# Performance work log

Hardware: AMD Instinct MI355X
Metric: run time of the kernel (lower is better)

Reference implementation:

```python
import jax, jax.numpy as jnp
import numpy as np

B, T, C, D = 4, 2048, 1024, 64


def setup_inputs() -> dict:
    key = jax.random.key(0)
    k_x, k_wq, k_wk, k_wv, k_b = jax.random.split(key, 5)
    s = 1.0 / np.sqrt(C)
    return {
        "hidden_states": jax.random.normal(k_x, (B, T, C), dtype=jnp.float32),
        "w_q": jax.random.normal(k_wq, (C, D), dtype=jnp.float32) * s,
        "w_k": jax.random.normal(k_wk, (C, D), dtype=jnp.float32) * s,
        "w_v": jax.random.normal(k_wv, (C, D), dtype=jnp.float32) * s,
        "b_q": jnp.zeros((D,), dtype=jnp.float32),
        "b_k": jnp.zeros((D,), dtype=jnp.float32),
        "b_v": jnp.zeros((D,), dtype=jnp.float32),
    }


def reference(hidden_states, w_q, w_k, w_v, b_q, b_k, b_v):
    # Single causal self-attention head (dropout = 0 / eval mode).
    q = hidden_states @ w_q + b_q                      # (B, T, D)
    k = hidden_states @ w_k + b_k                      # (B, T, D)
    v = hidden_states @ w_v + b_v                      # (B, T, D)
    scores = jnp.einsum("btd,bsd->bts", q, k) / jnp.sqrt(jnp.float32(D))
    t = hidden_states.shape[1]
    causal = jnp.tril(jnp.ones((t, t), dtype=bool))    # (T, T)
    scores = jnp.where(causal, scores, jnp.float32(-jnp.inf))
    weights = jax.nn.softmax(scores, axis=-1)          # (B, T, T)
    return jnp.einsum("bts,bsd->btd", weights, v)      # (B, T, D)
```

## Files before the change

### kernel.cpp

```cpp
#include <hip/hip_runtime.h>
#include <hip/hip_bf16.h>

constexpr int Bn = 4;
constexpr int Tn = 2048;
constexpr int Cn = 1024;
constexpr int Dn = 64;

typedef __attribute__((ext_vector_type(8))) short short8;
typedef __attribute__((ext_vector_type(4))) float f32x4;

__device__ inline short f2bf(float f) {
    unsigned u = __builtin_bit_cast(unsigned, f);
    u += 0x7FFFu + ((u >> 16) & 1u);
    return (short)(u >> 16);
}

__global__ __launch_bounds__(256) void prep_w(
    const float* __restrict__ wq, const float* __restrict__ wk,
    const float* __restrict__ wv, short* __restrict__ wt)
{
    const int sel = blockIdx.x >> 4;
    const float* w = sel == 0 ? wq : (sel == 1 ? wk : wv);
    short* o = wt + (size_t)sel * Dn * Cn;
    const int base = (blockIdx.x & 15) * 4096;
    for (int idx = base + threadIdx.x; idx < base + 4096; idx += 256) {
        int n = idx >> 10, k = idx & 1023;
        o[idx] = f2bf(w[k * Dn + n]);
    }
}

__global__ __launch_bounds__(64) void qkv_mfma(
    const float* __restrict__ x, const short* __restrict__ wt,
    const float* __restrict__ bq, const float* __restrict__ bk,
    const float* __restrict__ bv,
    short* __restrict__ Qbf, short* __restrict__ Kbf, short* __restrict__ Vt)
{
    const int l = threadIdx.x;
    const int i = l & 15, g = l >> 4;
    const int rowbase = blockIdx.x * 16;
    const int sel = blockIdx.y;

    const short* ws   = wt + (size_t)sel * Dn * Cn;
    const float* bias = sel == 0 ? bq : (sel == 1 ? bk : bv);

    f32x4 acc[4];
    #pragma unroll
    for (int nt = 0; nt < 4; ++nt)
        #pragma unroll
        for (int r = 0; r < 4; ++r) acc[nt][r] = 0.f;

    const float* xrow = x + (size_t)(rowbase + i) * Cn;

    for (int k0 = 0; k0 < Cn; k0 += 32) {
        float4 x0 = *reinterpret_cast<const float4*>(xrow + k0 + 8 * g);
        float4 x1 = *reinterpret_cast<const float4*>(xrow + k0 + 8 * g + 4);
        short8 af;
        af[0] = f2bf(x0.x); af[1] = f2bf(x0.y); af[2] = f2bf(x0.z); af[3] = f2bf(x0.w);
        af[4] = f2bf(x1.x); af[5] = f2bf(x1.y); af[6] = f2bf(x1.z); af[7] = f2bf(x1.w);
        #pragma unroll
        for (int nt = 0; nt < 4; ++nt) {
            short8 bf = *reinterpret_cast<const short8*>(
                ws + (size_t)(nt * 16 + i) * Cn + k0 + 8 * g);
            acc[nt] = __builtin_amdgcn_mfma_f32_16x16x32_bf16(af, bf, acc[nt], 0, 0, 0);
        }
    }

    #pragma unroll
    for (int r = 0; r < 4; ++r) {
        const int rho = rowbase + 4 * g + r;
        const int b = rho >> 11, t = rho & (Tn - 1);
        #pragma unroll
        for (int nt = 0; nt < 4; ++nt) {
            const int n = nt * 16 + i;
            const float val = acc[nt][r] + bias[n];
            if (sel == 0)      Qbf[(size_t)rho * Dn + n] = f2bf(val * 0.125f);
            else if (sel == 1) Kbf[(size_t)rho * Dn + n] = f2bf(val);
            else               Vt[((size_t)b * Dn + n) * Tn + t] = f2bf(val);
        }
    }
}

__global__ __launch_bounds__(256) void attn_fused(
    const short* __restrict__ Qbf, const short* __restrict__ Kbf,
    const short* __restrict__ Vt, float* __restrict__ out)
{
    __shared__ __align__(16) short Plds[4][16][72];
    __shared__ float o_part[4][16][68];
    __shared__ float ml_part[4][2][16];

    const int tid = threadIdx.x;
    const int w = tid >> 6, l = tid & 63;
    const int i = l & 15, g = l >> 4;
    const int b = blockIdx.y;
    const int qw = blockIdx.x * 16;

    const short* Qb = Qbf + (size_t)b * Tn * Dn;
    const short* Kb = Kbf + (size_t)b * Tn * Dn;
    const short* Vb = Vt + (size_t)b * Dn * Tn;

    short8 qf0 = *reinterpret_cast<const short8*>(Qb + (size_t)(qw + i) * Dn + 8 * g);
    short8 qf1 = *reinterpret_cast<const short8*>(Qb + (size_t)(qw + i) * Dn + 32 + 8 * g);

    f32x4 o4[4];
    f32x4 m, lsum;
    #pragma unroll
    for (int r = 0; r < 4; ++r) { m[r] = -1e30f; lsum[r] = 0.f; }
    #pragma unroll
    for (int dt = 0; dt < 4; ++dt)
        #pragma unroll
        for (int r = 0; r < 4; ++r) o4[dt][r] = 0.f;

    const int nch = (qw + 79) >> 6;
    for (int kb = w; kb < nch; kb += 4) {
        const int K0 = kb * 64;

        f32x4 s[4];
        #pragma unroll
        for (int nt = 0; nt < 4; ++nt)
            #pragma unroll
            for (int r = 0; r < 4; ++r) s[nt][r] = 0.f;
        #pragma unroll
        for (int nt = 0; nt < 4; ++nt) {
            const short* kr = Kb + (size_t)(K0 + nt * 16 + i) * Dn + 8 * g;
            short8 kf0 = *reinterpret_cast<const short8*>(kr);
            short8 kf1 = *reinterpret_cast<const short8*>(kr + 32);
            s[nt] = __builtin_amdgcn_mfma_f32_16x16x32_bf16(qf0, kf0, s[nt], 0, 0, 0);
            s[nt] = __builtin_amdgcn_mfma_f32_16x16x32_bf16(qf1, kf1, s[nt], 0, 0, 0);
        }

        if (K0 + 63 > qw) {
            #pragma unroll
            for (int nt = 0; nt < 4; ++nt)
                #pragma unroll
                for (int r = 0; r < 4; ++r) {
                    if (K0 + nt * 16 + i > qw + 4 * g + r) s[nt][r] = -1e30f;
                }
        }

        f32x4 rm;
        #pragma unroll
        for (int r = 0; r < 4; ++r)
            rm[r] = fmaxf(fmaxf(s[0][r], s[1][r]), fmaxf(s[2][r], s[3][r]));
        #pragma unroll
        for (int msk = 1; msk < 16; msk <<= 1)
            #pragma unroll
            for (int r = 0; r < 4; ++r) rm[r] = fmaxf(rm[r], __shfl_xor(rm[r], msk));

        f32x4 scl;
        #pragma unroll
        for (int r = 0; r < 4; ++r) {
            float mn = fmaxf(m[r], rm[r]);
            scl[r] = __expf(m[r] - mn);
            m[r] = mn;
            lsum[r] *= scl[r];
        }
        #pragma unroll
        for (int dt = 0; dt < 4; ++dt)
            #pragma unroll
            for (int r = 0; r < 4; ++r) o4[dt][r] *= scl[r];

        f32x4 rs;
        #pragma unroll
        for (int r = 0; r < 4; ++r) rs[r] = 0.f;
        #pragma unroll
        for (int nt = 0; nt < 4; ++nt)
            #pragma unroll
            for (int r = 0; r < 4; ++r) {
                float p = __expf(s[nt][r] - m[r]);
                rs[r] += p;
                Plds[w][4 * g + r][nt * 16 + i] = f2bf(p);
            }
        #pragma unroll
        for (int msk = 1; msk < 16; msk <<= 1)
            #pragma unroll
            for (int r = 0; r < 4; ++r) rs[r] += __shfl_xor(rs[r], msk);
        #pragma unroll
        for (int r = 0; r < 4; ++r) lsum[r] += rs[r];

        asm volatile("s_waitcnt lgkmcnt(0)" ::: "memory");
        __builtin_amdgcn_sched_barrier(0);

        short8 pf0 = *reinterpret_cast<const short8*>(&Plds[w][i][8 * g]);
        short8 pf1 = *reinterpret_cast<const short8*>(&Plds[w][i][32 + 8 * g]);
        #pragma unroll
        for (int dt = 0; dt < 4; ++dt) {
            const short* vr = Vb + (size_t)(dt * 16 + i) * Tn + K0 + 8 * g;
            short8 vf0 = *reinterpret_cast<const short8*>(vr);
            short8 vf1 = *reinterpret_cast<const short8*>(vr + 32);
            o4[dt] = __builtin_amdgcn_mfma_f32_16x16x32_bf16(pf0, vf0, o4[dt], 0, 0, 0);
            o4[dt] = __builtin_amdgcn_mfma_f32_16x16x32_bf16(pf1, vf1, o4[dt], 0, 0, 0);
        }
    }

    #pragma unroll
    for (int dt = 0; dt < 4; ++dt)
        #pragma unroll
        for (int r = 0; r < 4; ++r)
            o_part[w][4 * g + r][dt * 16 + i] = o4[dt][r];
    if (i == 0) {
        #pragma unroll
        for (int r = 0; r < 4; ++r) {
            ml_part[w][0][4 * g + r] = m[r];
            ml_part[w][1][4 * g + r] = lsum[r];
        }
    }
    __syncthreads();

    #pragma unroll
    for (int r = 0; r < 4; ++r) {
        const int row = 4 * g + r;
        float m0 = ml_part[0][0][row], m1 = ml_part[1][0][row];
        float m2 = ml_part[2][0][row], m3 = ml_part[3][0][row];
        float M = fmaxf(fmaxf(m0, m1), fmaxf(m2, m3));
        float w0 = __expf(m0 - M), w1 = __expf(m1 - M);
        float w2 = __expf(m2 - M), w3 = __expf(m3 - M);
        float L = ml_part[0][1][row] * w0 + ml_part[1][1][row] * w1 +
                  ml_part[2][1][row] * w2 + ml_part[3][1][row] * w3;
        float O = o_part[0][row][w * 16 + i] * w0 + o_part[1][row][w * 16 + i] * w1 +
                  o_part[2][row][w * 16 + i] * w2 + o_part[3][row][w * 16 + i] * w3;
        out[((size_t)b * Tn + qw + row) * Dn + w * 16 + i] = O / L;
    }
}

extern "C" void kernel_launch(void* const* d_in, const int* in_sizes, int n_in,
                              void* d_out, int out_size, void* d_ws, size_t ws_size,
                              hipStream_t stream) {
    const float* x  = (const float*)d_in[0];
    const float* wq = (const float*)d_in[1];
    const float* wk = (const float*)d_in[2];
    const float* wv = (const float*)d_in[3];
    const float* bq = (const float*)d_in[4];
    const float* bk = (const float*)d_in[5];
    const float* bv = (const float*)d_in[6];
    float* out = (float*)d_out;

    short* wt  = (short*)d_ws;
    short* Qbf = wt + 3 * Dn * Cn;
    short* Kbf = Qbf + (size_t)Bn * Tn * Dn;
    short* Vt  = Kbf + (size_t)Bn * Tn * Dn;

    prep_w<<<48, 256, 0, stream>>>(wq, wk, wv, wt);
    qkv_mfma<<<dim3((Bn * Tn) / 16, 3), 64, 0, stream>>>(x, wt, bq, bk, bv, Qbf, Kbf, Vt);
    attn_fused<<<dim3(Tn / 16, Bn), 256, 0, stream>>>(Qbf, Kbf, Vt, out);
}
```

Baseline: 149.5 us.

## Pre-convert activations to bf16, split QKV over N, use 8 waves in attention

Adds a prep pass that converts the full hidden_states tensor to bf16 in a workspace buffer, so the QKV projection loads bf16 directly instead of converting fp32 per block. The QKV kernel gets a third grid dimension that splits the 64 output columns into two halves, doubling the block count. The attention kernel goes from 4 to 8 waves per block, each wave taking a strided share of key chunks, and merges 8 partial softmax states at the end. The bf16 copy costs an extra full read and write of x, and the 8-way split doubles shared memory use per block and adds merge work.

```diff
diff --git a/kernel.cpp b/kernel.cpp
--- a/kernel.cpp
+++ b/kernel.cpp
@@ -15,22 +15,38 @@
     return (short)(u >> 16);
 }
 
-__global__ __launch_bounds__(256) void prep_w(
+__global__ __launch_bounds__(256) void prep(
+    const float* __restrict__ x,
     const float* __restrict__ wq, const float* __restrict__ wk,
-    const float* __restrict__ wv, short* __restrict__ wt)
+    const float* __restrict__ wv,
+    short* __restrict__ wt, short* __restrict__ xbf)
 {
-    const int sel = blockIdx.x >> 4;
-    const float* w = sel == 0 ? wq : (sel == 1 ? wk : wv);
-    short* o = wt + (size_t)sel * Dn * Cn;
-    const int base = (blockIdx.x & 15) * 4096;
-    for (int idx = base + threadIdx.x; idx < base + 4096; idx += 256) {
-        int n = idx >> 10, k = idx & 1023;
-        o[idx] = f2bf(w[k * Dn + n]);
+    if (blockIdx.x < 48) {
+        const int sel = blockIdx.x >> 4;
+        const float* w = sel == 0 ? wq : (sel == 1 ? wk : wv);
+        short* o = wt + (size_t)sel * Dn * Cn;
+        const int base = (blockIdx.x & 15) * 4096;
+        for (int idx = base + threadIdx.x; idx < base + 4096; idx += 256) {
+            int n = idx >> 10, k = idx & 1023;
+            o[idx] = f2bf(w[k * Dn + n]);
+        }
+    } else {
+        const int idx = (blockIdx.x - 48) * 256 + threadIdx.x;
+        const float4* xf = reinterpret_cast<const float4*>(x);
+        short8* xo = reinterpret_cast<short8*>(xbf);
+        constexpr int NU = Bn * Tn * Cn / 8;
+        for (int u = idx; u < NU; u += 262144) {
+            float4 a = xf[2 * u], c = xf[2 * u + 1];
+            short8 o;
+            o[0] = f2bf(a.x); o[1] = f2bf(a.y); o[2] = f2bf(a.z); o[3] = f2bf(a.w);
+            o[4] = f2bf(c.x); o[5] = f2bf(c.y); o[6] = f2bf(c.z); o[7] = f2bf(c.w);
+            xo[u] = o;
+        }
     }
 }
 
 __global__ __launch_bounds__(64) void qkv_mfma(
-    const float* __restrict__ x, const short* __restrict__ wt,
+    const short* __restrict__ xbf, const short* __restrict__ wt,
     const float* __restrict__ bq, const float* __restrict__ bk,
     const float* __restrict__ bv,
     short* __restrict__ Qbf, short* __restrict__ Kbf, short* __restrict__ Vt)
@@ -39,30 +55,27 @@
     const int i = l & 15, g = l >> 4;
     const int rowbase = blockIdx.x * 16;
     const int sel = blockIdx.y;
+    const int nh = blockIdx.z;
 
     const short* ws   = wt + (size_t)sel * Dn * Cn;
     const float* bias = sel == 0 ? bq : (sel == 1 ? bk : bv);
 
-    f32x4 acc[4];
-    #pragma unroll
-    for (int nt = 0; nt < 4; ++nt)
-        #pragma unroll
-        for (int r = 0; r < 4; ++r) acc[nt][r] = 0.f;
-
-    const float* xrow = x + (size_t)(rowbase + i) * Cn;
+    f32x4 acc[2];
+    #pragma unroll
+    for (int nt2 = 0; nt2 < 2; ++nt2)
+        #pragma unroll
+        for (int r = 0; r < 4; ++r) acc[nt2][r] = 0.f;
+
+    const short* xrow = xbf + (size_t)(rowbase + i) * Cn + 8 * g;
+    const short* wb0  = ws + (size_t)(nh * 32 + i) * Cn + 8 * g;
+    const short* wb1  = wb0 + (size_t)16 * Cn;
 
     for (int k0 = 0; k0 < Cn; k0 += 32) {
-        float4 x0 = *reinterpret_cast<const float4*>(xrow + k0 + 8 * g);
-        float4 x1 = *reinterpret_cast<const float4*>(xrow + k0 + 8 * g + 4);
-        short8 af;
-        af[0] = f2bf(x0.x); af[1] = f2bf(x0.y); af[2] = f2bf(x0.z); af[3] = f2bf(x0.w);
-        af[4] = f2bf(x1.x); af[5] = f2bf(x1.y); af[6] = f2bf(x1.z); af[7] = f2bf(x1.w);
-        #pragma unroll
-        for (int nt = 0; nt < 4; ++nt) {
-            short8 bf = *reinterpret_cast<const short8*>(
-                ws + (size_t)(nt * 16 + i) * Cn + k0 + 8 * g);
-            acc[nt] = __builtin_amdgcn_mfma_f32_16x16x32_bf16(af, bf, acc[nt], 0, 0, 0);
-        }
+        short8 af = *reinterpret_cast<const short8*>(xrow + k0);
+        short8 b0 = *reinterpret_cast<const short8*>(wb0 + k0);
+        short8 b1 = *reinterpret_cast<const short8*>(wb1 + k0);
+        acc[0] = __builtin_amdgcn_mfma_f32_16x16x32_bf16(af, b0, acc[0], 0, 0, 0);
+        acc[1] = __builtin_amdgcn_mfma_f32_16x16x32_bf16(af, b1, acc[1], 0, 0, 0);
     }
 
     #pragma unroll
@@ -70,9 +83,9 @@
         const int rho = rowbase + 4 * g + r;
         const int b = rho >> 11, t = rho & (Tn - 1);
         #pragma unroll
-        for (int nt = 0; nt < 4; ++nt) {
-            const int n = nt * 16 + i;
-            const float val = acc[nt][r] + bias[n];
+        for (int nt2 = 0; nt2 < 2; ++nt2) {
+            const int n = (nh * 2 + nt2) * 16 + i;
+            const float val = acc[nt2][r] + bias[n];
             if (sel == 0)      Qbf[(size_t)rho * Dn + n] = f2bf(val * 0.125f);
             else if (sel == 1) Kbf[(size_t)rho * Dn + n] = f2bf(val);
             else               Vt[((size_t)b * Dn + n) * Tn + t] = f2bf(val);
@@ -80,13 +93,13 @@
     }
 }
 
-__global__ __launch_bounds__(256) void attn_fused(
+__global__ __launch_bounds__(512) void attn_fused(
     const short* __restrict__ Qbf, const short* __restrict__ Kbf,
     const short* __restrict__ Vt, float* __restrict__ out)
 {
-    __shared__ __align__(16) short Plds[4][16][72];
-    __shared__ float o_part[4][16][68];
-    __shared__ float ml_part[4][2][16];
+    __shared__ __align__(16) short Plds[8][16][72];
+    __shared__ float o_part[8][16][68];
+    __shared__ float ml_part[8][2][16];
 
     const int tid = threadIdx.x;
     const int w = tid >> 6, l = tid & 63;
@@ -111,7 +124,7 @@
         for (int r = 0; r < 4; ++r) o4[dt][r] = 0.f;
 
     const int nch = (qw + 79) >> 6;
-    for (int kb = w; kb < nch; kb += 4) {
+    for (int kb = w; kb < nch; kb += 8) {
         const int K0 = kb * 64;
 
         f32x4 s[4];
@@ -206,19 +219,22 @@
     }
     __syncthreads();
 
-    #pragma unroll
-    for (int r = 0; r < 4; ++r) {
-        const int row = 4 * g + r;
-        float m0 = ml_part[0][0][row], m1 = ml_part[1][0][row];
-        float m2 = ml_part[2][0][row], m3 = ml_part[3][0][row];
-        float M = fmaxf(fmaxf(m0, m1), fmaxf(m2, m3));
-        float w0 = __expf(m0 - M), w1 = __expf(m1 - M);
-        float w2 = __expf(m2 - M), w3 = __expf(m3 - M);
-        float L = ml_part[0][1][row] * w0 + ml_part[1][1][row] * w1 +
-                  ml_part[2][1][row] * w2 + ml_part[3][1][row] * w3;
-        float O = o_part[0][row][w * 16 + i] * w0 + o_part[1][row][w * 16 + i] * w1 +
-                  o_part[2][row][w * 16 + i] * w2 + o_part[3][row][w * 16 + i] * w3;
-        out[((size_t)b * Tn + qw + row) * Dn + w * 16 + i] = O / L;
+    if (w < 4) {
+        #pragma unroll
+        for (int r = 0; r < 4; ++r) {
+            const int row = 4 * g + r;
+            float M = -1e30f;
+            #pragma unroll
+            for (int p = 0; p < 8; ++p) M = fmaxf(M, ml_part[p][0][row]);
+            float L = 0.f, O = 0.f;
+            #pragma unroll
+            for (int p = 0; p < 8; ++p) {
+                float wp = __expf(ml_part[p][0][row] - M);
+                L += ml_part[p][1][row] * wp;
+                O += o_part[p][row][w * 16 + i] * wp;
+            }
+            out[((size_t)b * Tn + qw + row) * Dn + w * 16 + i] = O / L;
+        }
     }
 }
 
@@ -235,11 +251,13 @@
     float* out = (float*)d_out;
 
     short* wt  = (short*)d_ws;
-    short* Qbf = wt + 3 * Dn * Cn;
+    short* xbf = wt + 3 * Dn * Cn;
+    short* Qbf = xbf + (size_t)Bn * Tn * Cn;
     short* Kbf = Qbf + (size_t)Bn * Tn * Dn;
     short* Vt  = Kbf + (size_t)Bn * Tn * Dn;
 
-    prep_w<<<48, 256, 0, stream>>>(wq, wk, wv, wt);
-    qkv_mfma<<<dim3((Bn * Tn) / 16, 3), 64, 0, stream>>>(x, wt, bq, bk, bv, Qbf, Kbf, Vt);
-    attn_fused<<<dim3(Tn / 16, Bn), 256, 0, stream>>>(Qbf, Kbf, Vt, out);
-}
+    prep<<<1072, 256, 0, stream>>>(x, wq, wk, wv, wt, xbf);
+    qkv_mfma<<<dim3((Bn * Tn) / 16, 3, 2), 64, 0, stream>>>(
+        xbf, wt, bq, bk, bv, Qbf, Kbf, Vt);
+    attn_fused<<<dim3(Tn / 16, Bn), 512, 0, stream>>>(Qbf, Kbf, Vt, out);
+}
```

Result: slower. 156.2 us (+4.5%).

## Prefetch x in QKV projection, hoist V loads, and use 8 waves in attention

Applied to the files above, without the earlier changes.

The QKV projection kernel now double-buffers its fp32 input loads two k-steps ahead and fully unrolls the k loop, so global loads can overlap the MFMA work. The attention kernel doubles its block to 8 waves, giving each wave fewer key chunks. V fragments are loaded right after the QK MFMAs so their latency overlaps the softmax. The final merge now combines 8 partial results, with only the first 4 waves writing output. In exchange it uses more registers and LDS, which may lower occupancy, and adds reduction work per block.

```diff
diff --git a/kernel.cpp b/kernel.cpp
--- a/kernel.cpp
+++ b/kernel.cpp
@@ -49,11 +49,23 @@
         #pragma unroll
         for (int r = 0; r < 4; ++r) acc[nt][r] = 0.f;
 
-    const float* xrow = x + (size_t)(rowbase + i) * Cn;
-
+    const float* xrow = x + (size_t)(rowbase + i) * Cn + 8 * g;
+
+    float4 pa[2], pb[2];
+    pa[0] = *reinterpret_cast<const float4*>(xrow + 0);
+    pb[0] = *reinterpret_cast<const float4*>(xrow + 4);
+    pa[1] = *reinterpret_cast<const float4*>(xrow + 32);
+    pb[1] = *reinterpret_cast<const float4*>(xrow + 36);
+
+    #pragma unroll
     for (int k0 = 0; k0 < Cn; k0 += 32) {
-        float4 x0 = *reinterpret_cast<const float4*>(xrow + k0 + 8 * g);
-        float4 x1 = *reinterpret_cast<const float4*>(xrow + k0 + 8 * g + 4);
+        const int s = (k0 >> 5) & 1;
+        float4 x0 = pa[s], x1 = pb[s];
+        const int kn = k0 + 64;
+        if (kn < Cn) {
+            pa[s] = *reinterpret_cast<const float4*>(xrow + kn);
+            pb[s] = *reinterpret_cast<const float4*>(xrow + kn + 4);
+        }
         short8 af;
         af[0] = f2bf(x0.x); af[1] = f2bf(x0.y); af[2] = f2bf(x0.z); af[3] = f2bf(x0.w);
         af[4] = f2bf(x1.x); af[5] = f2bf(x1.y); af[6] = f2bf(x1.z); af[7] = f2bf(x1.w);
@@ -80,13 +92,13 @@
     }
 }
 
-__global__ __launch_bounds__(256) void attn_fused(
+__global__ __launch_bounds__(512) void attn_fused(
     const short* __restrict__ Qbf, const short* __restrict__ Kbf,
     const short* __restrict__ Vt, float* __restrict__ out)
 {
-    __shared__ __align__(16) short Plds[4][16][72];
-    __shared__ float o_part[4][16][68];
-    __shared__ float ml_part[4][2][16];
+    __shared__ __align__(16) short Plds[8][16][72];
+    __shared__ float o_part[8][16][68];
+    __shared__ float ml_part[8][2][16];
 
     const int tid = threadIdx.x;
     const int w = tid >> 6, l = tid & 63;
@@ -111,7 +123,7 @@
         for (int r = 0; r < 4; ++r) o4[dt][r] = 0.f;
 
     const int nch = (qw + 79) >> 6;
-    for (int kb = w; kb < nch; kb += 4) {
+    for (int kb = w; kb < nch; kb += 8) {
         const int K0 = kb * 64;
 
         f32x4 s[4];
@@ -128,6 +140,14 @@
             s[nt] = __builtin_amdgcn_mfma_f32_16x16x32_bf16(qf1, kf1, s[nt], 0, 0, 0);
         }
 
+        short8 vf0[4], vf1[4];
+        #pragma unroll
+        for (int dt = 0; dt < 4; ++dt) {
+            const short* vr = Vb + (size_t)(dt * 16 + i) * Tn + K0 + 8 * g;
+            vf0[dt] = *reinterpret_cast<const short8*>(vr);
+            vf1[dt] = *reinterpret_cast<const short8*>(vr + 32);
+        }
+
         if (K0 + 63 > qw) {
             #pragma unroll
             for (int nt = 0; nt < 4; ++nt)
@@ -184,11 +204,8 @@
         short8 pf1 = *reinterpret_cast<const short8*>(&Plds[w][i][32 + 8 * g]);
         #pragma unroll
         for (int dt = 0; dt < 4; ++dt) {
-            const short* vr = Vb + (size_t)(dt * 16 + i) * Tn + K0 + 8 * g;
-            short8 vf0 = *reinterpret_cast<const short8*>(vr);
-            short8 vf1 = *reinterpret_cast<const short8*>(vr + 32);
-            o4[dt] = __builtin_amdgcn_mfma_f32_16x16x32_bf16(pf0, vf0, o4[dt], 0, 0, 0);
-            o4[dt] = __builtin_amdgcn_mfma_f32_16x16x32_bf16(pf1, vf1, o4[dt], 0, 0, 0);
+            o4[dt] = __builtin_amdgcn_mfma_f32_16x16x32_bf16(pf0, vf0[dt], o4[dt], 0, 0, 0);
+            o4[dt] = __builtin_amdgcn_mfma_f32_16x16x32_bf16(pf1, vf1[dt], o4[dt], 0, 0, 0);
         }
     }
 
@@ -206,19 +223,22 @@
     }
     __syncthreads();
 
-    #pragma unroll
-    for (int r = 0; r < 4; ++r) {
-        const int row = 4 * g + r;
-        float m0 = ml_part[0][0][row], m1 = ml_part[1][0][row];
-        float m2 = ml_part[2][0][row], m3 = ml_part[3][0][row];
-        float M = fmaxf(fmaxf(m0, m1), fmaxf(m2, m3));
-        float w0 = __expf(m0 - M), w1 = __expf(m1 - M);
-        float w2 = __expf(m2 - M), w3 = __expf(m3 - M);
-        float L = ml_part[0][1][row] * w0 + ml_part[1][1][row] * w1 +
-                  ml_part[2][1][row] * w2 + ml_part[3][1][row] * w3;
-        float O = o_part[0][row][w * 16 + i] * w0 + o_part[1][row][w * 16 + i] * w1 +
-                  o_part[2][row][w * 16 + i] * w2 + o_part[3][row][w * 16 + i] * w3;
-        out[((size_t)b * Tn + qw + row) * Dn + w * 16 + i] = O / L;
+    if (w < 4) {
+        #pragma unroll
+        for (int r = 0; r < 4; ++r) {
+            const int row = 4 * g + r;
+            float M = -1e30f;
+            #pragma unroll
+            for (int p = 0; p < 8; ++p) M = fmaxf(M, ml_part[p][0][row]);
+            float L = 0.f, O = 0.f;
+            #pragma unroll
+            for (int p = 0; p < 8; ++p) {
+                float wp = __expf(ml_part[p][0][row] - M);
+                L += ml_part[p][1][row] * wp;
+                O += o_part[p][row][w * 16 + i] * wp;
+            }
+            out[((size_t)b * Tn + qw + row) * Dn + w * 16 + i] = O / L;
+        }
     }
 }
 
@@ -240,6 +260,7 @@
     short* Vt  = Kbf + (size_t)Bn * Tn * Dn;
 
     prep_w<<<48, 256, 0, stream>>>(wq, wk, wv, wt);
-    qkv_mfma<<<dim3((Bn * Tn) / 16, 3), 64, 0, stream>>>(x, wt, bq, bk, bv, Qbf, Kbf, Vt);
-    attn_fused<<<dim3(Tn / 16, Bn), 256, 0, stream>>>(Qbf, Kbf, Vt, out);
-}
+    qkv_mfma<<<dim3((Bn * Tn) / 16, 3), 64, 0, stream>>>(
+        x, wt, bq, bk, bv, Qbf, Kbf, Vt);
+    attn_fused<<<dim3(Tn / 16, Bn), 512, 0, stream>>>(Qbf, Kbf, Vt, out);
+}
```

After: 149.4 us. Within noise of the previous version (-0.0%).
